# Kernel tuning notes

Measured on AMD Instinct MI355X. Metric: run time of the kernel, lower is better.

The kernel has to match this reference:

```python
import jax, jax.numpy as jnp
import numpy as np

COMMITMENT_COST = 0.25


def setup_inputs() -> dict:
    key = jax.random.key(0)
    k1, k2 = jax.random.split(key)
    x = jax.random.normal(k1, (32, 128, 32, 32), dtype=jnp.float32)
    num_embeddings, embedding_dim = 512, 128
    # torch init: uniform(-1/num_embeddings, 1/num_embeddings)
    lim = 1.0 / num_embeddings
    emb = jax.random.uniform(k2, (num_embeddings, embedding_dim),
                             minval=-lim, maxval=lim, dtype=jnp.float32)
    return {"x": x, "emb": emb}


def reference(x, emb):
    B, C, H, W = x.shape
    K = emb.shape[0]
    # flatten to [N, C] in (B,H,W) order
    flat = jnp.transpose(x, (0, 2, 3, 1)).reshape(-1, C)
    # squared L2 distances: ||f||^2 + ||e||^2 - 2 f.e
    distances = ((flat * flat).sum(axis=1, keepdims=True)
                 + (emb * emb).sum(axis=1)
                 - 2.0 * jnp.matmul(flat, emb.T))  # [N, K]
    indices = jnp.argmin(distances, axis=1)  # [N]
    quantized = emb[indices].reshape(B, H, W, C).transpose(0, 3, 1, 2)  # [B,C,H,W]
    e_latent_loss = jnp.mean((jax.lax.stop_gradient(quantized) - x) ** 2)
    q_latent_loss = jnp.mean((quantized - jax.lax.stop_gradient(x)) ** 2)
    vq_loss = q_latent_loss + COMMITMENT_COST * e_latent_loss
    # straight-through estimator
    quantized_st = x + jax.lax.stop_gradient(quantized - x)
    # codebook usage fraction (jit-friendly replacement for torch.unique)
    used = jnp.zeros((K,), dtype=jnp.float32).at[indices].set(1.0)
    usage = used.sum() / K
    return quantized_st, vq_loss, indices.reshape(B, H, W), usage
```

## Files before the change

kernel.cpp:

```cpp
#include <hip/hip_runtime.h>
#include <hip/hip_bf16.h>


#define NPOS   32768
#define KCODES 512
#define DCH    128
#define NELEM  4194304

#define OFF_LOSS  4194304
#define OFF_IDX   4194305
#define OFF_USAGE 4227073

__device__ __forceinline__ float round_barrier(float v) {
    asm volatile("" : "+v"(v));
    return v;
}


__global__ __launch_bounds__(512) void vq_prep(const float* __restrict__ emb,
                                               float* __restrict__ esq,
                                               int* __restrict__ flags) {
    int k = threadIdx.x;
    const float* row = emb + (size_t)k * DCH;
    float r[8];
#pragma unroll
    for (int j = 0; j < 8; ++j) {
        float v = row[j];
        r[j] = round_barrier(v * v);
    }
#pragma unroll
    for (int i = 8; i < DCH; i += 8) {
#pragma unroll
        for (int j = 0; j < 8; ++j) {
            float v = row[i + j];
            float sq = round_barrier(v * v);
            r[j] += sq;
        }
    }
    esq[k] = ((r[0] + r[1]) + (r[2] + r[3])) + ((r[4] + r[5]) + (r[6] + r[7]));
    flags[k] = 0;
}

__global__ __launch_bounds__(256) void vq_argmin(const float* __restrict__ x,
                                                 const float* __restrict__ emb,
                                                 const float* __restrict__ esq,
                                                 int* __restrict__ ws_idx,
                                                 int* __restrict__ flags,
                                                 float* __restrict__ out_idx) {
    __shared__ float xt[DCH][64];
    __shared__ float et[DCH][64];
    __shared__ float red_d[16][64];
    __shared__ int   red_i[16][64];
    __shared__ float sfsq[64];

    const int t   = threadIdx.x;
    const int n0  = blockIdx.x * 64;
    const int b   = n0 >> 10;
    const int hw0 = n0 & 1023;

    {
        const int cg = t >> 4;
        const int p4 = (t & 15) * 4;
#pragma unroll
        for (int it = 0; it < 8; ++it) {
            int c = it * 16 + cg;
            float4 v = *reinterpret_cast<const float4*>(
                x + (size_t)(b * DCH + c) * 1024 + hw0 + p4);
            *reinterpret_cast<float4*>(&xt[c][p4]) = v;
        }
    }
    __syncthreads();

    if (t < 64) {
        float r[8];
#pragma unroll
        for (int j = 0; j < 8; ++j) {
            float v = xt[j][t];
            r[j] = round_barrier(v * v);
        }
#pragma unroll
        for (int i = 8; i < DCH; i += 8) {
#pragma unroll
            for (int j = 0; j < 8; ++j) {
                float v = xt[i + j][t];
                float sq = round_barrier(v * v);
                r[j] += sq;
            }
        }
        sfsq[t] = ((r[0] + r[1]) + (r[2] + r[3])) + ((r[4] + r[5]) + (r[6] + r[7]));
    }
    __syncthreads();

    const int ty = t >> 4;
    const int tx = t & 15;

    float fsqr[4];
#pragma unroll
    for (int i = 0; i < 4; ++i) fsqr[i] = sfsq[ty * 4 + i];

    float best_d[4];
    int   best_i[4];
#pragma unroll
    for (int i = 0; i < 4; ++i) { best_d[i] = 3.4e38f; best_i[i] = 0; }

    for (int ch = 0; ch < 8; ++ch) {
        if (ch) __syncthreads();

        {
            const int kk = t >> 2;
            const int j  = t & 3;
            const float* row = emb + (size_t)(ch * 64 + kk) * DCH;
#pragma unroll
            for (int r = 0; r < 8; ++r) {
                int c0 = j * 32 + r * 4;
                float4 v = *reinterpret_cast<const float4*>(row + c0);
                et[c0 + 0][kk] = v.x;
                et[c0 + 1][kk] = v.y;
                et[c0 + 2][kk] = v.z;
                et[c0 + 3][kk] = v.w;
            }
        }
        __syncthreads();

        float acc[4][4];
#pragma unroll
        for (int i = 0; i < 4; ++i)
#pragma unroll
            for (int j = 0; j < 4; ++j) acc[i][j] = 0.f;

#pragma unroll 4
        for (int c = 0; c < DCH; ++c) {
            float4 xv = *reinterpret_cast<const float4*>(&xt[c][ty * 4]);
            float4 ev = *reinterpret_cast<const float4*>(&et[c][tx * 4]);
            float xa[4] = {xv.x, xv.y, xv.z, xv.w};
            float ea[4] = {ev.x, ev.y, ev.z, ev.w};
#pragma unroll
            for (int i = 0; i < 4; ++i)
#pragma unroll
                for (int j = 0; j < 4; ++j)
                    acc[i][j] = __builtin_fmaf(xa[i], ea[j], acc[i][j]);
        }

#pragma unroll
        for (int j = 0; j < 4; ++j) {
            int kg = ch * 64 + tx * 4 + j;
            float eq = esq[kg];
#pragma unroll
            for (int i = 0; i < 4; ++i) {
                float A = fsqr[i] + eq;
                float s = A - 2.f * acc[i][j];
                if (s < best_d[i]) { best_d[i] = s; best_i[i] = kg; }
            }
        }
    }

#pragma unroll
    for (int i = 0; i < 4; ++i) {
        red_d[tx][ty * 4 + i] = best_d[i];
        red_i[tx][ty * 4 + i] = best_i[i];
    }
    __syncthreads();

    if (t < 64) {
        int p = t;
        float bd = red_d[0][p];
        int   bi = red_i[0][p];
#pragma unroll
        for (int q = 1; q < 16; ++q) {
            float d = red_d[q][p];
            int   i = red_i[q][p];
            if (d < bd || (d == bd && i < bi)) { bd = d; bi = i; }
        }
        int n = n0 + p;
        ws_idx[n]  = bi;
        out_idx[n] = (float)bi;
        flags[bi]  = 1;
    }
}

__global__ __launch_bounds__(256) void vq_gather(const float* __restrict__ x,
                                                 const float* __restrict__ emb,
                                                 const int* __restrict__ ws_idx,
                                                 float* __restrict__ out0,
                                                 double* __restrict__ partials) {
    __shared__ double sd[256];
    const int t = threadIdx.x;
    double local = 0.0;
    for (int e = blockIdx.x * 256 + t; e < NELEM; e += 2048 * 256) {
        int bc = e >> 10;
        int hw = e & 1023;
        int c  = bc & 127;
        int bb = bc >> 7;
        int n  = bb * 1024 + hw;
        int idx = ws_idx[n];
        float q  = emb[(size_t)idx * DCH + c];
        float xv = x[e];
        float dq = q - xv;
        out0[e] = xv + dq;
        local += (double)(dq * dq);
    }
    sd[t] = local;
    __syncthreads();
    for (int s = 128; s > 0; s >>= 1) {
        if (t < s) sd[t] += sd[t + s];
        __syncthreads();
    }
    if (t == 0) partials[blockIdx.x] = sd[0];
}

__global__ __launch_bounds__(512) void vq_final(const double* __restrict__ partials,
                                                const int* __restrict__ flags,
                                                float* __restrict__ out_loss,
                                                float* __restrict__ out_usage) {
    __shared__ double sd[512];
    __shared__ int    si[512];
    const int t = threadIdx.x;
    double s = 0.0;
    for (int i = t; i < 2048; i += 512) s += partials[i];
    sd[t] = s;
    si[t] = flags[t];
    __syncthreads();
    for (int k = 256; k > 0; k >>= 1) {
        if (t < k) { sd[t] += sd[t + k]; si[t] += si[t + k]; }
        __syncthreads();
    }
    if (t == 0) {
        float m = (float)(sd[0] / (double)NELEM);
        *out_loss  = m + 0.25f * m;
        *out_usage = (float)si[0] / (float)KCODES;
    }
}

extern "C" void kernel_launch(void* const* d_in, const int* in_sizes, int n_in,
                              void* d_out, int out_size, void* d_ws, size_t ws_size,
                              hipStream_t stream) {
    const float* x   = (const float*)d_in[0];
    const float* emb = (const float*)d_in[1];
    float* out = (float*)d_out;

    float* out0      = out;
    float* out_loss  = out + OFF_LOSS;
    float* out_idx   = out + OFF_IDX;
    float* out_usage = out + OFF_USAGE;

    char* ws = (char*)d_ws;
    int*    ws_idx   = (int*)ws;
    int*    ws_flags = (int*)(ws + 131072);
    float*  ws_esq   = (float*)(ws + 133120);
    double* ws_part  = (double*)(ws + 135168);

    vq_prep  <<<1,    512, 0, stream>>>(emb, ws_esq, ws_flags);
    vq_argmin<<<512,  256, 0, stream>>>(x, emb, ws_esq, ws_idx, ws_flags, out_idx);
    vq_gather<<<2048, 256, 0, stream>>>(x, emb, ws_idx, out0, ws_part);
    vq_final <<<1,    512, 0, stream>>>(ws_part, ws_flags, out_loss, out_usage);
}
```

Baseline: 126.9 us.

## Fuse argmin and gather into one kernel with larger per-thread tiles

```diff
diff --git a/kernel.cpp b/kernel.cpp
--- a/kernel.cpp
+++ b/kernel.cpp
@@ -2,20 +2,21 @@
 #include <hip/hip_bf16.h>
 
 
-#define NPOS   32768
+#define DCH    128
 #define KCODES 512
-#define DCH    128
 #define NELEM  4194304
+#define POSB   32
+#define NBLK   1024
 
 #define OFF_LOSS  4194304
 #define OFF_IDX   4194305
 #define OFF_USAGE 4227073
 
+
 __device__ __forceinline__ float round_barrier(float v) {
     asm volatile("" : "+v"(v));
     return v;
 }
-
 
 __global__ __launch_bounds__(512) void vq_prep(const float* __restrict__ emb,
                                                float* __restrict__ esq,
@@ -24,10 +25,7 @@
     const float* row = emb + (size_t)k * DCH;
     float r[8];
 #pragma unroll
-    for (int j = 0; j < 8; ++j) {
-        float v = row[j];
-        r[j] = round_barrier(v * v);
-    }
+    for (int j = 0; j < 8; ++j) { float v = row[j]; r[j] = round_barrier(v * v); }
 #pragma unroll
     for (int i = 8; i < DCH; i += 8) {
 #pragma unroll
@@ -41,164 +39,160 @@
     flags[k] = 0;
 }
 
-__global__ __launch_bounds__(256) void vq_argmin(const float* __restrict__ x,
-                                                 const float* __restrict__ emb,
-                                                 const float* __restrict__ esq,
-                                                 int* __restrict__ ws_idx,
-                                                 int* __restrict__ flags,
-                                                 float* __restrict__ out_idx) {
-    __shared__ float xt[DCH][64];
-    __shared__ float et[DCH][64];
-    __shared__ float red_d[16][64];
-    __shared__ int   red_i[16][64];
-    __shared__ float sfsq[64];
+__global__ __launch_bounds__(256, 4) void vq_main(const float* __restrict__ x,
+                                                  const float* __restrict__ emb,
+                                                  const float* __restrict__ esq,
+                                                  int* __restrict__ flags,
+                                                  float* __restrict__ out0,
+                                                  float* __restrict__ out_idx,
+                                                  double* __restrict__ partials) {
+    __shared__ __align__(16) float xt[16][32];
+    __shared__ __align__(16) float et[16][512];
+    __shared__ float esq_s[KCODES];
+    __shared__ float sfsq[POSB];
+    __shared__ int   sbi[POSB];
 
     const int t   = threadIdx.x;
-    const int n0  = blockIdx.x * 64;
+    const int n0  = blockIdx.x * POSB;
     const int b   = n0 >> 10;
     const int hw0 = n0 & 1023;
+    const float* xb = x + (size_t)b * DCH * 1024 + hw0;
+
+    esq_s[t]       = esq[t];
+    esq_s[t + 256] = esq[t + 256];
 
     {
-        const int cg = t >> 4;
-        const int p4 = (t & 15) * 4;
-#pragma unroll
-        for (int it = 0; it < 8; ++it) {
-            int c = it * 16 + cg;
+        const int p = t >> 3, j = t & 7;
+        float r;
+        {
+            float v = xb[(size_t)j * 1024 + p];
+            r = round_barrier(v * v);
+        }
+#pragma unroll
+        for (int i = 1; i < 16; ++i) {
+            float v = xb[(size_t)(8 * i + j) * 1024 + p];
+            float sq = round_barrier(v * v);
+            r += sq;
+        }
+        float (*sr)[POSB] = (float (*)[POSB]) & et[0][0];
+        sr[j][p] = r;
+    }
+    __syncthreads();
+    if (t < POSB) {
+        float (*sr)[POSB] = (float (*)[POSB]) & et[0][0];
+        sfsq[t] = ((sr[0][t] + sr[1][t]) + (sr[2][t] + sr[3][t]))
+                + ((sr[4][t] + sr[5][t]) + (sr[6][t] + sr[7][t]));
+    }
+
+    const int ty = t >> 6;
+    const int tx = t & 63;
+
+    float acc[8][8];
+#pragma unroll
+    for (int i = 0; i < 8; ++i)
+#pragma unroll
+        for (int j = 0; j < 8; ++j) acc[i][j] = 0.f;
+
+    const int kst = t >> 2;
+    const int jst = t & 3;
+
+    for (int cc = 0; cc < 8; ++cc) {
+        __syncthreads();
+
+        {
+            const int cl = t >> 4;
+            const int p2 = (t & 15) * 2;
+            float2 v = *reinterpret_cast<const float2*>(
+                xb + (size_t)(cc * 16 + cl) * 1024 + p2);
+            *reinterpret_cast<float2*>(&xt[cl][p2]) = v;
+        }
+#pragma unroll
+        for (int r = 0; r < 8; ++r) {
+            const int k = kst + 64 * r;
             float4 v = *reinterpret_cast<const float4*>(
-                x + (size_t)(b * DCH + c) * 1024 + hw0 + p4);
-            *reinterpret_cast<float4*>(&xt[c][p4]) = v;
-        }
-    }
-    __syncthreads();
-
-    if (t < 64) {
-        float r[8];
-#pragma unroll
-        for (int j = 0; j < 8; ++j) {
-            float v = xt[j][t];
-            r[j] = round_barrier(v * v);
-        }
-#pragma unroll
-        for (int i = 8; i < DCH; i += 8) {
-#pragma unroll
-            for (int j = 0; j < 8; ++j) {
-                float v = xt[i + j][t];
-                float sq = round_barrier(v * v);
-                r[j] += sq;
-            }
-        }
-        sfsq[t] = ((r[0] + r[1]) + (r[2] + r[3])) + ((r[4] + r[5]) + (r[6] + r[7]));
-    }
-    __syncthreads();
-
-    const int ty = t >> 4;
-    const int tx = t & 15;
-
-    float fsqr[4];
-#pragma unroll
-    for (int i = 0; i < 4; ++i) fsqr[i] = sfsq[ty * 4 + i];
-
-    float best_d[4];
-    int   best_i[4];
-#pragma unroll
-    for (int i = 0; i < 4; ++i) { best_d[i] = 3.4e38f; best_i[i] = 0; }
-
-    for (int ch = 0; ch < 8; ++ch) {
-        if (ch) __syncthreads();
-
-        {
-            const int kk = t >> 2;
-            const int j  = t & 3;
-            const float* row = emb + (size_t)(ch * 64 + kk) * DCH;
-#pragma unroll
-            for (int r = 0; r < 8; ++r) {
-                int c0 = j * 32 + r * 4;
-                float4 v = *reinterpret_cast<const float4*>(row + c0);
-                et[c0 + 0][kk] = v.x;
-                et[c0 + 1][kk] = v.y;
-                et[c0 + 2][kk] = v.z;
-                et[c0 + 3][kk] = v.w;
-            }
-        }
-        __syncthreads();
-
-        float acc[4][4];
-#pragma unroll
-        for (int i = 0; i < 4; ++i)
-#pragma unroll
-            for (int j = 0; j < 4; ++j) acc[i][j] = 0.f;
-
-#pragma unroll 4
-        for (int c = 0; c < DCH; ++c) {
-            float4 xv = *reinterpret_cast<const float4*>(&xt[c][ty * 4]);
-            float4 ev = *reinterpret_cast<const float4*>(&et[c][tx * 4]);
-            float xa[4] = {xv.x, xv.y, xv.z, xv.w};
-            float ea[4] = {ev.x, ev.y, ev.z, ev.w};
-#pragma unroll
-            for (int i = 0; i < 4; ++i)
-#pragma unroll
-                for (int j = 0; j < 4; ++j)
+                emb + (size_t)k * DCH + cc * 16 + jst * 4);
+            et[jst * 4 + 0][k] = v.x;
+            et[jst * 4 + 1][k] = v.y;
+            et[jst * 4 + 2][k] = v.z;
+            et[jst * 4 + 3][k] = v.w;
+        }
+        __syncthreads();
+
+#pragma unroll
+        for (int cl = 0; cl < 16; ++cl) {
+            float4 xv0 = *reinterpret_cast<const float4*>(&xt[cl][ty * 8]);
+            float4 xv1 = *reinterpret_cast<const float4*>(&xt[cl][ty * 8 + 4]);
+            float4 ev0 = *reinterpret_cast<const float4*>(&et[cl][tx * 8]);
+            float4 ev1 = *reinterpret_cast<const float4*>(&et[cl][tx * 8 + 4]);
+            float xa[8] = {xv0.x, xv0.y, xv0.z, xv0.w, xv1.x, xv1.y, xv1.z, xv1.w};
+            float ea[8] = {ev0.x, ev0.y, ev0.z, ev0.w, ev1.x, ev1.y, ev1.z, ev1.w};
+#pragma unroll
+            for (int i = 0; i < 8; ++i)
+#pragma unroll
+                for (int j = 0; j < 8; ++j)
                     acc[i][j] = __builtin_fmaf(xa[i], ea[j], acc[i][j]);
         }
-
-#pragma unroll
-        for (int j = 0; j < 4; ++j) {
-            int kg = ch * 64 + tx * 4 + j;
-            float eq = esq[kg];
-#pragma unroll
-            for (int i = 0; i < 4; ++i) {
-                float A = fsqr[i] + eq;
-                float s = A - 2.f * acc[i][j];
-                if (s < best_d[i]) { best_d[i] = s; best_i[i] = kg; }
-            }
-        }
-    }
-
-#pragma unroll
-    for (int i = 0; i < 4; ++i) {
-        red_d[tx][ty * 4 + i] = best_d[i];
-        red_i[tx][ty * 4 + i] = best_i[i];
-    }
-    __syncthreads();
-
-    if (t < 64) {
-        int p = t;
-        float bd = red_d[0][p];
-        int   bi = red_i[0][p];
-#pragma unroll
-        for (int q = 1; q < 16; ++q) {
-            float d = red_d[q][p];
-            int   i = red_i[q][p];
-            if (d < bd || (d == bd && i < bi)) { bd = d; bi = i; }
-        }
-        int n = n0 + p;
-        ws_idx[n]  = bi;
-        out_idx[n] = (float)bi;
-        flags[bi]  = 1;
-    }
-}
-
-__global__ __launch_bounds__(256) void vq_gather(const float* __restrict__ x,
-                                                 const float* __restrict__ emb,
-                                                 const int* __restrict__ ws_idx,
-                                                 float* __restrict__ out0,
-                                                 double* __restrict__ partials) {
-    __shared__ double sd[256];
-    const int t = threadIdx.x;
+    }
+
+    float bd[8];
+    int   bi[8];
+#pragma unroll
+    for (int i = 0; i < 8; ++i) { bd[i] = 3.4e38f; bi[i] = 0; }
+#pragma unroll
+    for (int j = 0; j < 8; ++j) {
+        const int kg = tx * 8 + j;
+        const float eq = esq_s[kg];
+#pragma unroll
+        for (int i = 0; i < 8; ++i) {
+            float A = sfsq[ty * 8 + i] + eq;
+            float s = A - 2.f * acc[i][j];
+            if (s < bd[i]) { bd[i] = s; bi[i] = kg; }
+        }
+    }
+#pragma unroll
+    for (int m = 1; m < 64; m <<= 1) {
+#pragma unroll
+        for (int i = 0; i < 8; ++i) {
+            float d2 = __shfl_xor(bd[i], m, 64);
+            int   i2 = __shfl_xor(bi[i], m, 64);
+            if (d2 < bd[i] || (d2 == bd[i] && i2 < bi[i])) { bd[i] = d2; bi[i] = i2; }
+        }
+    }
+    if (tx == 0) {
+#pragma unroll
+        for (int i = 0; i < 8; ++i) {
+            const int p = ty * 8 + i;
+            out_idx[n0 + p] = (float)bi[i];
+            sbi[p] = bi[i];
+            flags[bi[i]] = 1;
+        }
+    }
+    __syncthreads();
+
     double local = 0.0;
-    for (int e = blockIdx.x * 256 + t; e < NELEM; e += 2048 * 256) {
-        int bc = e >> 10;
-        int hw = e & 1023;
-        int c  = bc & 127;
-        int bb = bc >> 7;
-        int n  = bb * 1024 + hw;
-        int idx = ws_idx[n];
-        float q  = emb[(size_t)idx * DCH + c];
-        float xv = x[e];
-        float dq = q - xv;
-        out0[e] = xv + dq;
-        local += (double)(dq * dq);
-    }
+    {
+        const int cl8 = t >> 3;
+        const int p4  = (t & 7) * 4;
+        const int i0 = sbi[p4], i1 = sbi[p4 + 1], i2 = sbi[p4 + 2], i3 = sbi[p4 + 3];
+#pragma unroll
+        for (int it = 0; it < 4; ++it) {
+            const int c = it * 32 + cl8;
+            float4 xv = *reinterpret_cast<const float4*>(xb + (size_t)c * 1024 + p4);
+            float q0 = emb[(size_t)i0 * DCH + c];
+            float q1 = emb[(size_t)i1 * DCH + c];
+            float q2 = emb[(size_t)i2 * DCH + c];
+            float q3 = emb[(size_t)i3 * DCH + c];
+            float d0 = q0 - xv.x, d1 = q1 - xv.y, d2 = q2 - xv.z, d3 = q3 - xv.w;
+            float4 o = {xv.x + d0, xv.y + d1, xv.z + d2, xv.w + d3};
+            *reinterpret_cast<float4*>(
+                out0 + (size_t)(b * DCH + c) * 1024 + hw0 + p4) = o;
+            local += (double)(d0 * d0);
+            local += (double)(d1 * d1);
+            local += (double)(d2 * d2);
+            local += (double)(d3 * d3);
+        }
+    }
+    double* sd = reinterpret_cast<double*>(&et[0][0]);
     sd[t] = local;
     __syncthreads();
     for (int s = 128; s > 0; s >>= 1) {
@@ -215,8 +209,7 @@
     __shared__ double sd[512];
     __shared__ int    si[512];
     const int t = threadIdx.x;
-    double s = 0.0;
-    for (int i = t; i < 2048; i += 512) s += partials[i];
+    double s = partials[t] + partials[t + 512];
     sd[t] = s;
     si[t] = flags[t];
     __syncthreads();
@@ -244,13 +237,11 @@
     float* out_usage = out + OFF_USAGE;
 
     char* ws = (char*)d_ws;
-    int*    ws_idx   = (int*)ws;
-    int*    ws_flags = (int*)(ws + 131072);
-    float*  ws_esq   = (float*)(ws + 133120);
-    double* ws_part  = (double*)(ws + 135168);
-
-    vq_prep  <<<1,    512, 0, stream>>>(emb, ws_esq, ws_flags);
-    vq_argmin<<<512,  256, 0, stream>>>(x, emb, ws_esq, ws_idx, ws_flags, out_idx);
-    vq_gather<<<2048, 256, 0, stream>>>(x, emb, ws_idx, out0, ws_part);
-    vq_final <<<1,    512, 0, stream>>>(ws_part, ws_flags, out_loss, out_usage);
-}
+    int*    ws_flags = (int*)ws;
+    float*  ws_esq   = (float*)(ws + 2048);
+    double* ws_part  = (double*)(ws + 4096);
+
+    vq_prep <<<1,    512, 0, stream>>>(emb, ws_esq, ws_flags);
+    vq_main <<<NBLK, 256, 0, stream>>>(x, emb, ws_esq, ws_flags, out0, out_idx, ws_part);
+    vq_final<<<1,    512, 0, stream>>>(ws_part, ws_flags, out_loss, out_usage);
+}
```

Result: faster. 108.0 us (-14.9%).
